# Optimization experiments

Hardware: AMD Instinct MI355X
Metric: run time of the kernel (lower is better)

## Reference

```python
import jax, jax.numpy as jnp
import numpy as np

B, T, D, H = 2, 2048, 2048, 16
HD = D // H
SCALE = HD ** -0.5
NEG_INF = float('-inf')


def setup_inputs() -> dict:
    key = jax.random.key(0)
    ks = jax.random.split(key, 10)
    x = jax.random.normal(ks[0], (B, T, D), dtype=jnp.float32)
    # causal float mask: 0 on/below diagonal, -inf above (broadcast over B, H)
    causal = jnp.triu(jnp.ones((T, T), dtype=bool), k=1)
    mask = jnp.where(causal, NEG_INF, 0.0).astype(jnp.float32)[None, None]
    # xavier_uniform for [D, D]: bound = sqrt(6 / (D + D))
    bound = float(np.sqrt(6.0 / (D + D)))
    def xav(k):
        return jax.random.uniform(k, (D, D), jnp.float32, -bound, bound)
    wq, wk, wv, wo = xav(ks[1]), xav(ks[2]), xav(ks[3]), xav(ks[4])
    # biases: uniform_[0,1)
    bq = jax.random.uniform(ks[5], (D,), jnp.float32)
    bk = jax.random.uniform(ks[6], (D,), jnp.float32)
    bv = jax.random.uniform(ks[7], (D,), jnp.float32)
    bo = jax.random.uniform(ks[8], (D,), jnp.float32)
    return {"x": x, "mask": mask, "wq": wq, "bq": bq, "wk": wk, "bk": bk,
            "wv": wv, "bv": bv, "wo": wo, "bo": bo}


def reference(x, mask, wq, bq, wk, bk, wv, bv, wo, bo):
    b, t, d = x.shape
    def split_heads(y):  # [B,T,D] -> [B,H,T,HD]
        return y.reshape(b, t, H, HD).transpose(0, 2, 1, 3)
    q = split_heads(x @ wq.T + bq)
    k = split_heads(x @ wk.T + bk)
    v = split_heads(x @ wv.T + bv)
    scores = jnp.einsum('bhqd,bhkd->bhqk', q, k) * SCALE
    scores = jnp.where(mask == NEG_INF, NEG_INF, scores)
    attn = jax.nn.softmax(scores, axis=-1)
    out = jnp.einsum('bhqk,bhkd->bhqd', attn, v)  # [B,H,T,HD]
    out = out.transpose(0, 2, 1, 3).reshape(b, t, d)
    return out @ wo.T + bo
```

## Files before the change

kernel.cpp:

```cpp
#include <hip/hip_runtime.h>

typedef unsigned short u16;
typedef __bf16 bf16x8 __attribute__((ext_vector_type(8)));
typedef float f32x4 __attribute__((ext_vector_type(4)));

constexpr int B_ = 2, T_ = 2048, D_ = 2048, H_ = 16, HD_ = 128;
constexpr int MROWS = B_ * T_;
constexpr int KD = D_;
constexpr int ND = D_;
#define SL2E (0.08838834764831845f * 1.4426950408889634f)

__device__ __forceinline__ u16 f2bf(float f) {
  unsigned u = __float_as_uint(f);
  u += 0x7FFF + ((u >> 16) & 1);
  return (u16)(u >> 16);
}

__device__ __forceinline__ float fexp2(float x) { return __builtin_amdgcn_exp2f(x); }

__device__ __forceinline__ void async16(const void* g, void* l) {
  __builtin_amdgcn_global_load_lds((__attribute__((address_space(1))) void*)g,
                                   (__attribute__((address_space(3))) void*)l,
                                   16, 0, 0);
}

__global__ void cvt_kernel(const float* __restrict__ in, u16* __restrict__ out, int n) {
  int i = (blockIdx.x * blockDim.x + threadIdx.x) * 4;
  if (i >= n) return;
  const float4 v = *(const float4*)(in + i);
  ushort4 h;
  h.x = f2bf(v.x); h.y = f2bf(v.y); h.z = f2bf(v.z); h.w = f2bf(v.w);
  *(ushort4*)(out + i) = h;
}

__global__ void cvt4_kernel(const float* __restrict__ w0, const float* __restrict__ w1,
                            const float* __restrict__ w2, const float* __restrict__ w3,
                            u16* __restrict__ o0, u16* __restrict__ o1,
                            u16* __restrict__ o2, u16* __restrict__ o3, int n) {
  const float* in = blockIdx.y == 0 ? w0 : blockIdx.y == 1 ? w1 : blockIdx.y == 2 ? w2 : w3;
  u16* out = blockIdx.y == 0 ? o0 : blockIdx.y == 1 ? o1 : blockIdx.y == 2 ? o2 : o3;
  int i = (blockIdx.x * blockDim.x + threadIdx.x) * 4;
  if (i >= n) return;
  const float4 v = *(const float4*)(in + i);
  ushort4 h;
  h.x = f2bf(v.x); h.y = f2bf(v.y); h.z = f2bf(v.z); h.w = f2bf(v.w);
  *(ushort4*)(out + i) = h;
}

template <int MODE>
__device__ __forceinline__ void gemm_body(const u16* __restrict__ A,
                                          const u16* __restrict__ Bw,
                                          const float* __restrict__ bias,
                                          void* __restrict__ outp,
                                          u16* As, u16* Bs) {
  constexpr int BK = 32;
  const int tid = threadIdx.x;
  const int wave = tid >> 6;
  const int lane = tid & 63;
  const int quad = lane >> 4;
  const int l16 = lane & 15;
  const int wm = (wave >> 1) * 64;
  const int wn = (wave & 1) * 64;
  const int mBase = blockIdx.y * 128;
  const int nBase = blockIdx.x * 128;

  f32x4 acc[4][4] = {};

  const int srow = wave * 32 + (lane >> 2);
  const int soff = (lane & 3) * 8;
  const u16* Ag = A + (size_t)(mBase + srow) * KD + soff;
  const u16* Bg = Bw + (size_t)(nBase + srow) * KD + soff;
  u16* AsW0 = &As[(wave * 32) * BK];
  u16* AsW1 = &As[(wave * 32 + 16) * BK];
  u16* BsW0 = &Bs[(wave * 32) * BK];
  u16* BsW1 = &Bs[(wave * 32 + 16) * BK];

  for (int k0 = 0; k0 < KD; k0 += BK) {
    __syncthreads();
    async16(Ag + k0, AsW0);
    async16(Ag + 16 * KD + k0, AsW1);
    async16(Bg + k0, BsW0);
    async16(Bg + 16 * KD + k0, BsW1);
    __syncthreads();

    bf16x8 a[4], b[4];
#pragma unroll
    for (int i = 0; i < 4; i++)
      a[i] = *(const bf16x8*)&As[(wm + i * 16 + l16) * BK + quad * 8];
#pragma unroll
    for (int j = 0; j < 4; j++)
      b[j] = *(const bf16x8*)&Bs[(wn + j * 16 + l16) * BK + quad * 8];
#pragma unroll
    for (int i = 0; i < 4; i++)
#pragma unroll
      for (int j = 0; j < 4; j++)
        acc[i][j] = __builtin_amdgcn_mfma_f32_16x16x32_bf16(a[i], b[j], acc[i][j], 0, 0, 0);
  }

  float* outF = (float*)outp;
  u16* outH = (u16*)outp;
#pragma unroll
  for (int i = 0; i < 4; i++) {
#pragma unroll
    for (int j = 0; j < 4; j++) {
      const int col = nBase + wn + j * 16 + l16;
      const float bv = bias[col];
#pragma unroll
      for (int r = 0; r < 4; r++) {
        const int row = mBase + wm + i * 16 + quad * 4 + r;
        const float v = acc[i][j][r] + bv;
        if (MODE == 0) {
          outH[(size_t)row * ND + col] = f2bf(v);
        } else if (MODE == 1) {
          const int bb = row >> 11;
          const int t = row & (T_ - 1);
          const int h = col >> 7;
          const int d = col & (HD_ - 1);
          outH[(size_t)(((bb * H_ + h) << 7) + d) * T_ + t] = f2bf(v);
        } else {
          outF[(size_t)row * ND + col] = v;
        }
      }
    }
  }
}

__global__ __launch_bounds__(256) void gemm_qkv(const u16* __restrict__ A,
                                                const u16* __restrict__ Wq, const u16* __restrict__ Wk,
                                                const u16* __restrict__ Wv,
                                                const float* __restrict__ bq, const float* __restrict__ bk,
                                                const float* __restrict__ bv,
                                                u16* __restrict__ Qo, u16* __restrict__ Ko,
                                                u16* __restrict__ Vo) {
  __shared__ u16 As[128 * 32];
  __shared__ u16 Bs[128 * 32];
  const int z = blockIdx.z;
  const u16* Bw = z == 0 ? Wq : z == 1 ? Wk : Wv;
  const float* bias = z == 0 ? bq : z == 1 ? bk : bv;
  if (z == 2)
    gemm_body<1>(A, Bw, bias, (void*)Vo, As, Bs);
  else
    gemm_body<0>(A, Bw, bias, (void*)(z == 0 ? Qo : Ko), As, Bs);
}

__global__ __launch_bounds__(256) void gemm_out(const u16* __restrict__ A, const u16* __restrict__ Bw,
                                                const float* __restrict__ bias, float* __restrict__ outp) {
  __shared__ u16 As[128 * 32];
  __shared__ u16 Bs[128 * 32];
  gemm_body<2>(A, Bw, bias, (void*)outp, As, Bs);
}

constexpr int KSTR = 136;
constexpr int VSTR = 72;

__global__ __launch_bounds__(256) void attn_kernel(const u16* __restrict__ Q,
                                                   const u16* __restrict__ Kc,
                                                   const u16* __restrict__ Vt,
                                                   u16* __restrict__ O) {
  __shared__ u16 Ks[64 * KSTR];
  __shared__ u16 Vs[128 * VSTR];
  __shared__ u16 Ps[4 * 16 * VSTR];
  const int tid = threadIdx.x;
  const int wave = tid >> 6;
  const int lane = tid & 63;
  const int quad = lane >> 4;
  const int l16 = lane & 15;
  const int lo = blockIdx.x;
  const int hi = 31 - lo;
  const int bh = blockIdx.y;
  const int b = bh >> 4;
  const int h = bh & 15;

  const int tIdx[2] = {lo, hi};

  bf16x8 qf[2][4];
#pragma unroll
  for (int t = 0; t < 2; t++) {
    const u16* Qp = Q + (size_t)(b * T_ + tIdx[t] * 64 + wave * 16 + l16) * D_ + h * HD_;
#pragma unroll
    for (int kc = 0; kc < 4; kc++)
      qf[t][kc] = *(const bf16x8*)(Qp + kc * 32 + quad * 8);
  }

  f32x4 o[2][8] = {};
  float mrow[2][4], lrow[2][4];
#pragma unroll
  for (int t = 0; t < 2; t++)
#pragma unroll
    for (int r = 0; r < 4; r++) { mrow[t][r] = -__builtin_huge_valf(); lrow[t][r] = 0.f; }

  const u16* Kg = Kc + (size_t)(b * T_) * D_ + h * HD_;
  const u16* Vg = Vt + (size_t)((b * H_ + h) * HD_) * T_;
  u16* Pw = &Ps[wave * 16 * VSTR];

  for (int kt = 0; kt <= hi; kt++) {
    __syncthreads();
    {
      uint4 kv[4], vv[4];
      const int krow = tid >> 4, kc16 = tid & 15;
      const int vrow = tid >> 3, vc16 = tid & 7;
#pragma unroll
      for (int rr = 0; rr < 4; rr++)
        kv[rr] = *(const uint4*)(Kg + (size_t)(kt * 64 + rr * 16 + krow) * D_ + kc16 * 8);
#pragma unroll
      for (int rr = 0; rr < 4; rr++)
        vv[rr] = *(const uint4*)(Vg + (size_t)(rr * 32 + vrow) * T_ + kt * 64 + vc16 * 8);
#pragma unroll
      for (int rr = 0; rr < 4; rr++)
        *(uint4*)&Ks[(rr * 16 + krow) * KSTR + kc16 * 8] = kv[rr];
#pragma unroll
      for (int rr = 0; rr < 4; rr++)
        *(uint4*)&Vs[(rr * 32 + vrow) * VSTR + vc16 * 8] = vv[rr];
    }
    __syncthreads();

#pragma unroll
    for (int t = 0; t < 2; t++) {
      if (t == 0 && kt > lo) continue;
      const int qrow0 = tIdx[t] * 64 + wave * 16;

      f32x4 s[4];
#pragma unroll
      for (int nt = 0; nt < 4; nt++) {
        f32x4 a = {};
#pragma unroll
        for (int kc = 0; kc < 4; kc++) {
          bf16x8 kf = *(const bf16x8*)&Ks[(nt * 16 + l16) * KSTR + kc * 32 + quad * 8];
          a = __builtin_amdgcn_mfma_f32_16x16x32_bf16(qf[t][kc], kf, a, 0, 0, 0);
        }
        s[nt] = a;
      }

      const bool diag = (kt == tIdx[t]);
#pragma unroll
      for (int nt = 0; nt < 4; nt++)
#pragma unroll
        for (int r = 0; r < 4; r++) {
          float v = s[nt][r] * SL2E;
          if (diag) {
            const int colg = nt * 16 + l16;
            const int rowg = wave * 16 + quad * 4 + r;
            if (colg > rowg) v = -__builtin_huge_valf();
          }
          s[nt][r] = v;
        }

      float alpha[4];
#pragma unroll
      for (int r = 0; r < 4; r++) {
        float mx = fmaxf(fmaxf(s[0][r], s[1][r]), fmaxf(s[2][r], s[3][r]));
        mx = fmaxf(mx, __shfl_xor(mx, 1));
        mx = fmaxf(mx, __shfl_xor(mx, 2));
        mx = fmaxf(mx, __shfl_xor(mx, 4));
        mx = fmaxf(mx, __shfl_xor(mx, 8));
        const float mnew = fmaxf(mrow[t][r], mx);
        alpha[r] = fexp2(mrow[t][r] - mnew);
        mrow[t][r] = mnew;
        float sum = 0.f;
#pragma unroll
        for (int nt = 0; nt < 4; nt++) {
          const float p = fexp2(s[nt][r] - mnew);
          s[nt][r] = p;
          sum += p;
        }
        sum += __shfl_xor(sum, 1);
        sum += __shfl_xor(sum, 2);
        sum += __shfl_xor(sum, 4);
        sum += __shfl_xor(sum, 8);
        lrow[t][r] = lrow[t][r] * alpha[r] + sum;
      }

#pragma unroll
      for (int dt = 0; dt < 8; dt++)
#pragma unroll
        for (int r = 0; r < 4; r++)
          o[t][dt][r] *= alpha[r];

#pragma unroll
      for (int nt = 0; nt < 4; nt++)
#pragma unroll
        for (int r = 0; r < 4; r++)
          Pw[(quad * 4 + r) * VSTR + nt * 16 + l16] = f2bf(s[nt][r]);

      bf16x8 pf[2];
#pragma unroll
      for (int kc = 0; kc < 2; kc++)
        pf[kc] = *(const bf16x8*)&Pw[l16 * VSTR + kc * 32 + quad * 8];
#pragma unroll
      for (int dt = 0; dt < 8; dt++) {
#pragma unroll
        for (int kc = 0; kc < 2; kc++) {
          bf16x8 vf = *(const bf16x8*)&Vs[(dt * 16 + l16) * VSTR + kc * 32 + quad * 8];
          o[t][dt] = __builtin_amdgcn_mfma_f32_16x16x32_bf16(pf[kc], vf, o[t][dt], 0, 0, 0);
        }
      }
    }
  }

#pragma unroll
  for (int t = 0; t < 2; t++)
#pragma unroll
    for (int dt = 0; dt < 8; dt++)
#pragma unroll
      for (int r = 0; r < 4; r++) {
        const int rowg = b * T_ + tIdx[t] * 64 + wave * 16 + quad * 4 + r;
        const int col = h * HD_ + dt * 16 + l16;
        O[(size_t)rowg * D_ + col] = f2bf(o[t][dt][r] / lrow[t][r]);
      }
}

extern "C" void kernel_launch(void* const* d_in, const int* in_sizes, int n_in,
                              void* d_out, int out_size, void* d_ws, size_t ws_size,
                              hipStream_t stream) {
  (void)in_sizes; (void)n_in; (void)out_size; (void)ws_size;
  const float* x  = (const float*)d_in[0];
  const float* wq = (const float*)d_in[2];
  const float* bq = (const float*)d_in[3];
  const float* wk = (const float*)d_in[4];
  const float* bk = (const float*)d_in[5];
  const float* wv = (const float*)d_in[6];
  const float* bv = (const float*)d_in[7];
  const float* wo = (const float*)d_in[8];
  const float* bo = (const float*)d_in[9];

  u16* ws  = (u16*)d_ws;
  u16* xb  = ws;
  u16* wqb = ws + 8388608;
  u16* wkb = ws + 12582912;
  u16* wvb = ws + 16777216;
  u16* wob = ws + 20971520;
  u16* Qb  = ws + 25165824;
  u16* Kb  = ws + 33554432;
  u16* Vtb = ws + 41943040;
  u16* Ob  = ws + 50331648;

  cvt_kernel<<<8192, 256, 0, stream>>>(x, xb, 8388608);
  cvt4_kernel<<<dim3(4096, 4), 256, 0, stream>>>(wq, wk, wv, wo, wqb, wkb, wvb, wob, 4194304);

  dim3 gg(ND / 128, MROWS / 128, 3);
  gemm_qkv<<<gg, 256, 0, stream>>>(xb, wqb, wkb, wvb, bq, bk, bv, Qb, Kb, Vtb);
  attn_kernel<<<dim3(16, B_ * H_), 256, 0, stream>>>(Qb, Kb, Vtb, Ob);
  gemm_out<<<dim3(ND / 128, MROWS / 128), 256, 0, stream>>>(Ob, wob, bo, (float*)d_out);
}
```

Measured before the change: 412.3 us.

## Swizzle GEMM LDS tiles and transpose attention score layout for lane-local softmax

The GEMM now XOR-swizzles the 16-byte chunk offset used by the async global-to-LDS loads and by the fragment reads, to reduce LDS bank conflicts. In attention, QK^T is computed with the operands swapped, so each lane holds one query row's scores. Row max and sum then need two cross-lane shuffles instead of four per row, and P is written to LDS as packed 4-element stores. Rescale factors and the final normalizer are broadcast back with shuffles, and the final division becomes a multiply by the reciprocal.

```diff
diff --git a/kernel.cpp b/kernel.cpp
--- a/kernel.cpp
+++ b/kernel.cpp
@@ -67,13 +67,15 @@
   f32x4 acc[4][4] = {};
 
   const int srow = wave * 32 + (lane >> 2);
-  const int soff = (lane & 3) * 8;
+  const int soff = ((lane & 3) ^ ((lane >> 3) & 3)) * 8;
   const u16* Ag = A + (size_t)(mBase + srow) * KD + soff;
   const u16* Bg = Bw + (size_t)(nBase + srow) * KD + soff;
   u16* AsW0 = &As[(wave * 32) * BK];
   u16* AsW1 = &As[(wave * 32 + 16) * BK];
   u16* BsW0 = &Bs[(wave * 32) * BK];
   u16* BsW1 = &Bs[(wave * 32 + 16) * BK];
+
+  const int sw = (quad ^ ((l16 >> 1) & 3)) * 8;
 
   for (int k0 = 0; k0 < KD; k0 += BK) {
     __syncthreads();
@@ -86,10 +88,10 @@
     bf16x8 a[4], b[4];
 #pragma unroll
     for (int i = 0; i < 4; i++)
-      a[i] = *(const bf16x8*)&As[(wm + i * 16 + l16) * BK + quad * 8];
+      a[i] = *(const bf16x8*)&As[(wm + i * 16 + l16) * BK + sw];
 #pragma unroll
     for (int j = 0; j < 4; j++)
-      b[j] = *(const bf16x8*)&Bs[(wn + j * 16 + l16) * BK + quad * 8];
+      b[j] = *(const bf16x8*)&Bs[(wn + j * 16 + l16) * BK + sw];
 #pragma unroll
     for (int i = 0; i < 4; i++)
 #pragma unroll
@@ -183,11 +185,9 @@
   }
 
   f32x4 o[2][8] = {};
-  float mrow[2][4], lrow[2][4];
-#pragma unroll
-  for (int t = 0; t < 2; t++)
-#pragma unroll
-    for (int r = 0; r < 4; r++) { mrow[t][r] = -__builtin_huge_valf(); lrow[t][r] = 0.f; }
+  float mrow[2], lrow[2];
+#pragma unroll
+  for (int t = 0; t < 2; t++) { mrow[t] = -__builtin_huge_valf(); lrow[t] = 0.f; }
 
   const u16* Kg = Kc + (size_t)(b * T_) * D_ + h * HD_;
   const u16* Vg = Vt + (size_t)((b * H_ + h) * HD_) * T_;
@@ -217,18 +217,17 @@
 #pragma unroll
     for (int t = 0; t < 2; t++) {
       if (t == 0 && kt > lo) continue;
-      const int qrow0 = tIdx[t] * 64 + wave * 16;
-
-      f32x4 s[4];
+
+      f32x4 st[4];
 #pragma unroll
       for (int nt = 0; nt < 4; nt++) {
         f32x4 a = {};
 #pragma unroll
         for (int kc = 0; kc < 4; kc++) {
           bf16x8 kf = *(const bf16x8*)&Ks[(nt * 16 + l16) * KSTR + kc * 32 + quad * 8];
-          a = __builtin_amdgcn_mfma_f32_16x16x32_bf16(qf[t][kc], kf, a, 0, 0, 0);
-        }
-        s[nt] = a;
+          a = __builtin_amdgcn_mfma_f32_16x16x32_bf16(kf, qf[t][kc], a, 0, 0, 0);
+        }
+        st[nt] = a;
       }
 
       const bool diag = (kt == tIdx[t]);
@@ -236,51 +235,54 @@
       for (int nt = 0; nt < 4; nt++)
 #pragma unroll
         for (int r = 0; r < 4; r++) {
-          float v = s[nt][r] * SL2E;
+          float v = st[nt][r] * SL2E;
           if (diag) {
-            const int colg = nt * 16 + l16;
-            const int rowg = wave * 16 + quad * 4 + r;
-            if (colg > rowg) v = -__builtin_huge_valf();
+            const int kcol = nt * 16 + quad * 4 + r;
+            const int qrow = wave * 16 + l16;
+            if (kcol > qrow) v = -__builtin_huge_valf();
           }
-          s[nt][r] = v;
-        }
-
-      float alpha[4];
-#pragma unroll
-      for (int r = 0; r < 4; r++) {
-        float mx = fmaxf(fmaxf(s[0][r], s[1][r]), fmaxf(s[2][r], s[3][r]));
-        mx = fmaxf(mx, __shfl_xor(mx, 1));
-        mx = fmaxf(mx, __shfl_xor(mx, 2));
-        mx = fmaxf(mx, __shfl_xor(mx, 4));
-        mx = fmaxf(mx, __shfl_xor(mx, 8));
-        const float mnew = fmaxf(mrow[t][r], mx);
-        alpha[r] = fexp2(mrow[t][r] - mnew);
-        mrow[t][r] = mnew;
-        float sum = 0.f;
-#pragma unroll
-        for (int nt = 0; nt < 4; nt++) {
-          const float p = fexp2(s[nt][r] - mnew);
-          s[nt][r] = p;
+          st[nt][r] = v;
+        }
+
+      float mx = st[0][0];
+#pragma unroll
+      for (int nt = 0; nt < 4; nt++)
+#pragma unroll
+        for (int r = 0; r < 4; r++) mx = fmaxf(mx, st[nt][r]);
+      mx = fmaxf(mx, __shfl_xor(mx, 16));
+      mx = fmaxf(mx, __shfl_xor(mx, 32));
+      const float mnew = fmaxf(mrow[t], mx);
+      const float alpha = fexp2(mrow[t] - mnew);
+      mrow[t] = mnew;
+      float sum = 0.f;
+#pragma unroll
+      for (int nt = 0; nt < 4; nt++)
+#pragma unroll
+        for (int r = 0; r < 4; r++) {
+          const float p = fexp2(st[nt][r] - mnew);
+          st[nt][r] = p;
           sum += p;
         }
-        sum += __shfl_xor(sum, 1);
-        sum += __shfl_xor(sum, 2);
-        sum += __shfl_xor(sum, 4);
-        sum += __shfl_xor(sum, 8);
-        lrow[t][r] = lrow[t][r] * alpha[r] + sum;
-      }
-
+      sum += __shfl_xor(sum, 16);
+      sum += __shfl_xor(sum, 32);
+      lrow[t] = lrow[t] * alpha + sum;
+
+      float af[4];
+#pragma unroll
+      for (int r = 0; r < 4; r++) af[r] = __shfl(alpha, quad * 4 + r);
 #pragma unroll
       for (int dt = 0; dt < 8; dt++)
 #pragma unroll
         for (int r = 0; r < 4; r++)
-          o[t][dt][r] *= alpha[r];
-
-#pragma unroll
-      for (int nt = 0; nt < 4; nt++)
-#pragma unroll
-        for (int r = 0; r < 4; r++)
-          Pw[(quad * 4 + r) * VSTR + nt * 16 + l16] = f2bf(s[nt][r]);
+          o[t][dt][r] *= af[r];
+
+#pragma unroll
+      for (int nt = 0; nt < 4; nt++) {
+        ushort4 pk;
+        pk.x = f2bf(st[nt][0]); pk.y = f2bf(st[nt][1]);
+        pk.z = f2bf(st[nt][2]); pk.w = f2bf(st[nt][3]);
+        *(ushort4*)&Pw[l16 * VSTR + nt * 16 + quad * 4] = pk;
+      }
 
       bf16x8 pf[2];
 #pragma unroll
@@ -298,15 +300,19 @@
   }
 
 #pragma unroll
-  for (int t = 0; t < 2; t++)
+  for (int t = 0; t < 2; t++) {
+    float linv[4];
+#pragma unroll
+    for (int r = 0; r < 4; r++) linv[r] = 1.f / __shfl(lrow[t], quad * 4 + r);
 #pragma unroll
     for (int dt = 0; dt < 8; dt++)
 #pragma unroll
       for (int r = 0; r < 4; r++) {
         const int rowg = b * T_ + tIdx[t] * 64 + wave * 16 + quad * 4 + r;
         const int col = h * HD_ + dt * 16 + l16;
-        O[(size_t)rowg * D_ + col] = f2bf(o[t][dt][r] / lrow[t][r]);
-      }
+        O[(size_t)rowg * D_ + col] = f2bf(o[t][dt][r] * linv[r]);
+      }
+  }
 }
 
 extern "C" void kernel_launch(void* const* d_in, const int* in_sizes, int n_in,
```

Measured after the change: 403.5 us. -2.1%, faster.
